# Kernel tuning notes

Hardware: AMD Instinct MI355X
Metric: run time of the kernel (lower is better)

Reference implementation:

```python
import jax, jax.numpy as jnp
import numpy as np

DIM = 1024
HEADS = 16
DIM_HEAD = 64
SCALE = DIM_HEAD ** -0.5
LN_EPS = 1e-5


def layer_norm(x, g, b):
    mu = jnp.mean(x, axis=-1, keepdims=True)
    var = jnp.mean(jnp.square(x - mu), axis=-1, keepdims=True)
    return (x - mu) * jax.lax.rsqrt(var + LN_EPS) * g + b


def setup_inputs() -> dict:
    key = jax.random.key(0)
    ks = jax.random.split(key, 8)
    w_std = DIM ** -0.5  # keep GEMM outputs O(1)
    return {
        "query": jax.random.normal(ks[0], (4, 512, DIM), jnp.float32),
        "kv": jax.random.normal(ks[1], (4, 2048, DIM), jnp.float32),
        "ln_q_g": jnp.ones((DIM,), jnp.float32),
        "ln_q_b": jnp.zeros((DIM,), jnp.float32),
        "ln_kv_g": jnp.ones((DIM,), jnp.float32),
        "ln_kv_b": jnp.zeros((DIM,), jnp.float32),
        "Wq": jax.random.normal(ks[2], (DIM, DIM), jnp.float32) * w_std,
        "bq": jnp.zeros((DIM,), jnp.float32),
        "Wk": jax.random.normal(ks[3], (DIM, DIM), jnp.float32) * w_std,
        "bk": jnp.zeros((DIM,), jnp.float32),
        "Wv": jax.random.normal(ks[4], (DIM, DIM), jnp.float32) * w_std,
        "bv": jnp.zeros((DIM,), jnp.float32),
        "Wo": jax.random.normal(ks[5], (DIM, DIM), jnp.float32) * w_std,
        "bo": jnp.zeros((DIM,), jnp.float32),
    }


def reference(query, kv, ln_q_g, ln_q_b, ln_kv_g, ln_kv_b,
              Wq, bq, Wk, bk, Wv, bv, Wo, bo):
    kv_n = layer_norm(kv, ln_kv_g, ln_kv_b)            # (b, n_kv, d)
    residual = query
    q_n = layer_norm(query, ln_q_g, ln_q_b)            # (b, n_q, d)

    q = q_n @ Wq + bq                                   # (b, n_q, inner)
    kv_input = jnp.concatenate((kv_n, q_n), axis=-2)    # (b, n_kv+n_q, d)
    k = kv_input @ Wk + bk
    v = kv_input @ Wv + bv

    def split_heads(t):
        b, n, _ = t.shape
        return t.reshape(b, n, HEADS, DIM_HEAD).transpose(0, 2, 1, 3)  # b h n dh

    q = split_heads(q) * SCALE
    k = split_heads(k)
    v = split_heads(v)

    sim = jnp.einsum('bhid,bhjd->bhij', q, k)           # (b, h, n_q, n_kv+n_q)
    sim = sim - jax.lax.stop_gradient(jnp.max(sim, axis=-1, keepdims=True))
    attn = jax.nn.softmax(sim, axis=-1)
    out = jnp.einsum('bhij,bhjd->bhid', attn, v)        # (b, h, n_q, dh)

    b, h, n, dh = out.shape
    out = out.transpose(0, 2, 1, 3).reshape(b, n, h * dh)
    return out @ Wo + bo + residual
```

## Files before the change

### kernel.cpp

```cpp
#include <hip/hip_runtime.h>
#include <hip/hip_bf16.h>

#define B_    4
#define NQ    512
#define NKV   2048
#define NT    2560
#define DIM_  1024
#define HEADS 16
#define DH    64
#define NSEQT 10240
#define SCALE_Q_L2E 0.18033688011112042f

typedef short bf16x8 __attribute__((ext_vector_type(8)));
typedef float f32x4  __attribute__((ext_vector_type(4)));
typedef __hip_bfloat16 bf16;

__device__ inline void gll16(const bf16* g, bf16* l) {
  __builtin_amdgcn_global_load_lds(
      (const __attribute__((address_space(1))) unsigned int*)g,
      (__attribute__((address_space(3))) unsigned int*)l, 16, 0, 0);
}

#define VMCNT(n) asm volatile("s_waitcnt vmcnt(" #n ")" ::: "memory")
#define BAR() __builtin_amdgcn_s_barrier()

__global__ __launch_bounds__(256) void prep2_kernel(
    const float* __restrict__ query, const float* __restrict__ kv,
    const float* __restrict__ lgq, const float* __restrict__ lbq,
    const float* __restrict__ lgkv, const float* __restrict__ lbkv,
    bf16* __restrict__ X,
    const float* __restrict__ W0, const float* __restrict__ W1,
    const float* __restrict__ W2, const float* __restrict__ W3,
    bf16* __restrict__ T0, bf16* __restrict__ T1,
    bf16* __restrict__ T2, bf16* __restrict__ T3)
{
  __shared__ __align__(16) char psm[9216];
  const int t = threadIdx.x;
  const int blkid = blockIdx.x;
  if (blkid < 2560) {
    const int w = t>>6, l = t&63;
    const int R = blkid*4 + w;
    int b = R / NT, r = R % NT;
    const float *src, *gp, *bp;
    if (r < NKV) { src = kv    + ((size_t)b*NKV + r)*DIM_;      gp = lgkv; bp = lbkv; }
    else         { src = query + ((size_t)b*NQ + (r-NKV))*DIM_; gp = lgq;  bp = lbq;  }
    float4 v[4];
    #pragma unroll
    for (int j=0;j<4;++j) v[j] = ((const float4*)src)[j*64 + l];
    float s = 0.f, s2 = 0.f;
    #pragma unroll
    for (int j=0;j<4;++j){
      s  += v[j].x+v[j].y+v[j].z+v[j].w;
      s2 += v[j].x*v[j].x+v[j].y*v[j].y+v[j].z*v[j].z+v[j].w*v[j].w;
    }
    #pragma unroll
    for (int m=1;m<64;m<<=1){ s += __shfl_xor(s,m,64); s2 += __shfl_xor(s2,m,64); }
    float mu = s*(1.0f/DIM_);
    float rs = rsqrtf(s2*(1.0f/DIM_) - mu*mu + 1e-5f);
    uint2* drow = (uint2*)(X + (size_t)R*DIM_);
    #pragma unroll
    for (int j=0;j<4;++j){
      float4 gg = ((const float4*)gp)[j*64 + l];
      float4 b4 = ((const float4*)bp)[j*64 + l];
      union { unsigned int u[2]; bf16 h[4]; } pk;
      pk.h[0] = __float2bfloat16((v[j].x-mu)*rs*gg.x + b4.x);
      pk.h[1] = __float2bfloat16((v[j].y-mu)*rs*gg.y + b4.y);
      pk.h[2] = __float2bfloat16((v[j].z-mu)*rs*gg.z + b4.z);
      pk.h[3] = __float2bfloat16((v[j].w-mu)*rs*gg.w + b4.w);
      drow[j*64 + l] = make_uint2(pk.u[0], pk.u[1]);
    }
  } else {
    int l = blkid - 2560;
    const float* W; bf16* Wt;
    switch (l>>8) {
      case 0: W=W0; Wt=T0; break;
      case 1: W=W1; Wt=T1; break;
      case 2: W=W2; Wt=T2; break;
      default: W=W3; Wt=T3; break;
    }
    int rem = l & 255;
    int k0 = (rem&15)*64, n0 = (rem>>4)*64;
    bf16* Ws = (bf16*)psm;
    int kr = t>>2, nseg = (t&3)*16;
    const float4* s4 = (const float4*)(W + (size_t)(k0+kr)*DIM_ + n0 + nseg);
    union { uint4 u[2]; bf16 h[16]; } pk;
    #pragma unroll
    for (int j=0;j<4;j++){
      float4 v = s4[j];
      pk.h[j*4+0]=__float2bfloat16(v.x); pk.h[j*4+1]=__float2bfloat16(v.y);
      pk.h[j*4+2]=__float2bfloat16(v.z); pk.h[j*4+3]=__float2bfloat16(v.w);
    }
    *(uint4*)(Ws + kr*72 + nseg)     = pk.u[0];
    *(uint4*)(Ws + kr*72 + nseg + 8) = pk.u[1];
    __syncthreads();
    int n = t&63, kseg = t>>6;
    union { uint4 u[2]; bf16 h[16]; } o;
    #pragma unroll
    for (int k=0;k<16;k++) o.h[k] = Ws[(kseg*16+k)*72 + n];
    bf16* dst = Wt + (size_t)(n0+n)*DIM_ + k0 + kseg*16;
    *(uint4*)dst = o.u[0];
    *(uint4*)(dst+8) = o.u[1];
  }
}

__device__ __forceinline__ void gemm_core3(
    const bf16* __restrict__ A, const bf16* __restrict__ Bmat,
    const float* __restrict__ bias, const float* __restrict__ residual,
    void* __restrict__ outv, int rows_per_batch, int row_offset,
    int a_batch_stride_rows, int n_seq, float scale,
    int emode, int m0, int n0, char* smem)
{
  char* const sA = smem;
  char* const sB = smem + 24576;
  float* Ts = (float*)smem;

  const int t = threadIdx.x;
  const int lrow = t>>3, sl = t&7;
  const int sp   = sl ^ (lrow & 7);
  const int hsel = sp>>2, g = sp&3;
  const bf16 *pA[2], *pB[2];
  #pragma unroll
  for (int c = 0; c < 2; ++c) {
    int gm = m0 + 32*c + lrow + 64*hsel;
    int bi = gm / rows_per_batch;
    pA[c] = A + ((size_t)bi*a_batch_stride_rows + row_offset
                 + (gm - bi*rows_per_batch))*(size_t)DIM_ + g*8;
    int gn = n0 + 32*c + lrow + 64*hsel;
    pB[c] = Bmat + (size_t)gn*(size_t)DIM_ + g*8;
  }
  const int toff = t*16;

  const int wave = t>>6, lane = t&63, qq = lane>>4, mr = lane&15;
  const int wm = (wave>>1)*64, wn = (wave&1)*64;
  const int sAo = ((((wm>>6)<<2)|qq) ^ (mr&7))*16 + mr*128;
  const int sBo = ((((wn>>6)<<2)|qq) ^ (mr&7))*16 + mr*128;

  f32x4 acc[4][4] = {};

  #pragma unroll
  for (int p = 0; p < 2; ++p) {
    const int ko = p*32, bo = p*8192;
    gll16(pA[0]+ko, (bf16*)(sA + bo + toff));
    gll16(pA[1]+ko, (bf16*)(sA + bo + 4096 + toff));
    gll16(pB[0]+ko, (bf16*)(sB + bo + toff));
    gll16(pB[1]+ko, (bf16*)(sB + bo + 4096 + toff));
  }

  int rd = 0, wr2 = 2;
  for (int kt = 0; kt < 32; ++kt) {
    {
      const int kt2 = (kt+2 < 32) ? kt+2 : 31;
      const int ko = kt2*32, bo = wr2*8192;
      gll16(pA[0]+ko, (bf16*)(sA + bo + toff));
      gll16(pA[1]+ko, (bf16*)(sA + bo + 4096 + toff));
      gll16(pB[0]+ko, (bf16*)(sB + bo + toff));
      gll16(pB[1]+ko, (bf16*)(sB + bo + 4096 + toff));
    }
    VMCNT(8);
    BAR();
    {
      const char* Ab = sA + rd*8192;
      const char* Bb = sB + rd*8192;
      bf16x8 af[4], bfr[4];
      #pragma unroll
      for (int ms=0; ms<4; ++ms) af[ms]  = *(const bf16x8*)(Ab + ms*2048 + sAo);
      #pragma unroll
      for (int ns=0; ns<4; ++ns) bfr[ns] = *(const bf16x8*)(Bb + ns*2048 + sBo);
      __builtin_amdgcn_s_setprio(1);
      #pragma unroll
      for (int ms=0; ms<4; ++ms)
        #pragma unroll
        for (int ns=0; ns<4; ++ns)
          acc[ms][ns] = __builtin_amdgcn_mfma_f32_16x16x32_bf16(
              af[ms], bfr[ns], acc[ms][ns], 0,0,0);
      __builtin_amdgcn_s_setprio(0);
    }
    BAR();
    rd  = (rd  == 2) ? 0 : rd  + 1;
    wr2 = (wr2 == 2) ? 0 : wr2 + 1;
  }
  VMCNT(0);
  __syncthreads();

  const int lr = t>>3, cs = (t&7)*16;
  for (int R=0; R<4; R++){
    if ((wave>>1) == (R>>1)) {
      #pragma unroll
      for (int ms2=0; ms2<2; ms2++){
        int ms = (R&1)*2 + ms2;
        #pragma unroll
        for (int ns=0; ns<4; ns++){
          int col = wn + ns*16 + mr;
          #pragma unroll
          for (int r=0;r<4;r++)
            Ts[(ms2*16 + qq*4 + r)*132 + col] = acc[ms][ns][r];
        }
      }
    }
    __syncthreads();
    float v[16];
    #pragma unroll
    for (int j=0;j<4;j++){
      float4 f = *(const float4*)(Ts + lr*132 + cs + j*4);
      v[j*4+0]=f.x; v[j*4+1]=f.y; v[j*4+2]=f.z; v[j*4+3]=f.w;
    }
    int gr = m0 + R*32 + lr;
    int gc = n0 + cs;
    if (emode == 0) {
      float* out = (float*)outv;
      size_t base = (size_t)gr*DIM_ + gc;
      #pragma unroll
      for (int j=0;j<4;j++){
        float4 bv = *(const float4*)(bias + gc + j*4);
        float4 rv = *(const float4*)(residual + base + j*4);
        float4 o4;
        o4.x = v[j*4+0] + bv.x + rv.x;
        o4.y = v[j*4+1] + bv.y + rv.y;
        o4.z = v[j*4+2] + bv.z + rv.z;
        o4.w = v[j*4+3] + bv.w + rv.w;
        *(float4*)(out + base + j*4) = o4;
      }
    } else if (emode == 1) {
      int bb = gr / rows_per_batch;
      int n  = gr - bb*rows_per_batch;
      int hh = gc>>6, dh = gc&63;
      bf16* out = (bf16*)outv + ((size_t)(bb*HEADS + hh)*n_seq + n)*DH + dh;
      union { uint4 u[2]; bf16 h[16]; } pk;
      #pragma unroll
      for (int j=0;j<16;j++) pk.h[j] = __float2bfloat16((v[j] + bias[gc+j])*scale);
      *(uint4*)out     = pk.u[0];
      *(uint4*)(out+8) = pk.u[1];
    } else {
      float bc = bias[gr];
      bf16* out = (bf16*)outv + (size_t)gr*NSEQT + gc;
      union { uint4 u[2]; bf16 h[16]; } pk;
      #pragma unroll
      for (int j=0;j<16;j++) pk.h[j] = __float2bfloat16(v[j] + bc);
      *(uint4*)out     = pk.u[0];
      *(uint4*)(out+8) = pk.u[1];
    }
    __syncthreads();
  }
}

__global__ __launch_bounds__(256, 3) void gemm_qkv4(
    const bf16* __restrict__ X,
    const bf16* __restrict__ WtQ, const bf16* __restrict__ WtK,
    const bf16* __restrict__ WtV,
    const float* __restrict__ bq, const float* __restrict__ bk,
    const float* __restrict__ bv,
    bf16* __restrict__ Qhb, bf16* __restrict__ Khb, bf16* __restrict__ VTg)
{
  __shared__ __align__(16) char smem[49152];
  const int blk = blockIdx.x;
  if (blk < 128) {
    gemm_core3(X, WtQ, bq, nullptr, Qhb, NQ, NKV, NT, NQ, SCALE_Q_L2E, 1,
               (blk&15)*128, (blk>>4)*128, smem);
  } else if (blk < 768) {
    int l = blk - 128;
    gemm_core3(X, WtK, bk, nullptr, Khb, NT, 0, NT, NT, 1.0f, 1,
               (l%80)*128, (l/80)*128, smem);
  } else {
    int l = blk - 768;
    gemm_core3(WtV, X, bv, nullptr, VTg, DIM_, 0, DIM_, NSEQT, 1.0f, 2,
               (l/80)*128, (l%80)*128, smem);
  }
}

__global__ __launch_bounds__(256, 3) void gemm_o(
    const bf16* __restrict__ Ctx, const bf16* __restrict__ WtO,
    const float* __restrict__ bo, const float* __restrict__ residual,
    float* __restrict__ out)
{
  __shared__ __align__(16) char smem[49152];
  const int blk = blockIdx.x;
  gemm_core3(Ctx, WtO, bo, residual, out, B_*NQ, 0, B_*NQ, NQ, 1.0f, 0,
             (blk&15)*128, (blk>>4)*128, smem);
}

__global__ __launch_bounds__(256) void attn6_kernel(
    const bf16* __restrict__ Qh, const bf16* __restrict__ Kh,
    const bf16* __restrict__ VTg, bf16* __restrict__ Ctx)
{
  __shared__ __align__(16) bf16 KV[2][8192];
  __shared__ __align__(16) unsigned int Ps[4][640];

  const int t = threadIdx.x, wave = t>>6, lane = t&63;
  const int qq = lane>>4, mr = lane&15;
  const int blk = blockIdx.x;
  const int bh = (blk&7)*8 + (blk>>6);
  const int q0 = ((blk>>3)&7)*64;
  const int b = bh>>4, h = bh&15;
  const int pair = wave>>1, kh = wave&1;
  const int qb = pair*32;

  const int sl = t>>2, sc = t&3;
  const int skey = 32*(sl>>5) + 2*(sl&15) + ((sl>>4)&1);
  const bf16* Kb  = Kh + (size_t)bh*NT*DH + (size_t)skey*DH + sc*8;
  const bf16* VbT = VTg + ((size_t)(h*DH) + sl)*NSEQT + (size_t)b*NT + sc*8;

  bf16x8 qf[2][2];
  #pragma unroll
  for (int mt=0; mt<2; mt++){
    const bf16* Qb = Qh + ((size_t)bh*NQ + q0 + qb + mt*16 + mr)*DH;
    qf[mt][0] = *(const bf16x8*)(Qb + qq*8);
    qf[mt][1] = *(const bf16x8*)(Qb + 32 + qq*8);
  }

  f32x4 o[2][4] = {};
  float l[2][4] = {};
  unsigned int* Pw = &Ps[wave][0];

  {
    bf16* bp = &KV[0][0];
    gll16(Kb,        bp + t*8);
    gll16(Kb + 32,   bp + 2048 + t*8);
    gll16(VbT,       bp + 4096 + t*8);
    gll16(VbT + 32,  bp + 6144 + t*8);
  }

  for (int it = 0; it < NT/64; it++) {
    __syncthreads();
    if (it + 1 < NT/64) {
      int kt = (it+1)*64;
      bf16* bp = &KV[(it+1)&1][0];
      gll16(Kb  + (size_t)kt*DH,      bp + t*8);
      gll16(Kb  + (size_t)kt*DH + 32, bp + 2048 + t*8);
      gll16(VbT + kt,                 bp + 4096 + t*8);
      gll16(VbT + kt + 32,            bp + 6144 + t*8);
    }
    const bf16* cbuf = &KV[it&1][0];

    bf16x8 kf[2][2];
    #pragma unroll
    for (int g=0; g<2; g++){
      kf[g][0] = *(const bf16x8*)(cbuf + (32*kh + 16*g + mr)*32 + qq*8);
      kf[g][1] = *(const bf16x8*)(cbuf + 2048 + (32*kh + 16*g + mr)*32 + qq*8);
    }
    f32x4 s[2][2];
    #pragma unroll
    for (int mt=0; mt<2; mt++)
      #pragma unroll
      for (int g=0; g<2; g++){
        f32x4 z = {};
        z = __builtin_amdgcn_mfma_f32_16x16x32_bf16(qf[mt][0], kf[g][0], z, 0,0,0);
        z = __builtin_amdgcn_mfma_f32_16x16x32_bf16(qf[mt][1], kf[g][1], z, 0,0,0);
        s[mt][g] = z;
      }
    bf16x8 vf[4];
    #pragma unroll
    for (int n2=0; n2<4; n2++)
      vf[n2] = *(const bf16x8*)(cbuf + 4096 + kh*2048 + (n2*16+mr)*32 + qq*8);

    #pragma unroll
    for (int mt=0; mt<2; mt++)
      #pragma unroll
      for (int r=0; r<4; r++){
        float e0 = __builtin_amdgcn_exp2f(s[mt][0][r]);
        float e1 = __builtin_amdgcn_exp2f(s[mt][1][r]);
        l[mt][r] += e0 + e1;
        unsigned a0 = __float_as_uint(e0) + 0x8000u;
        unsigned a1 = __float_as_uint(e1) + 0x8000u;
        Pw[(mt*16 + qq*4 + r)*20 + mr] = __builtin_amdgcn_perm(a1, a0, 0x07060302u);
      }
    asm volatile("s_waitcnt lgkmcnt(0)" ::: "memory");
    bf16x8 pa[2];
    #pragma unroll
    for (int mt=0; mt<2; mt++)
      pa[mt] = *(const bf16x8*)(Pw + (mt*16+mr)*20 + qq*4);
    #pragma unroll
    for (int mt=0; mt<2; mt++)
      #pragma unroll
      for (int n2=0; n2<4; n2++)
        o[mt][n2] = __builtin_amdgcn_mfma_f32_16x16x32_bf16(pa[mt], vf[n2], o[mt][n2], 0,0,0);
  }

  float lsum[2][4];
  #pragma unroll
  for (int mt=0; mt<2; mt++)
    #pragma unroll
    for (int r=0; r<4; r++){
      float v = l[mt][r];
      #pragma unroll
      for (int m=1;m<16;m<<=1) v += __shfl_xor(v, m, 16);
      lsum[mt][r] = v;
    }

  __syncthreads();
  float* Of  = (float*)&KV[0][0];
  float* lsh = (float*)&Ps[0][0];
  if (kh == 1) {
    #pragma unroll
    for (int mt=0; mt<2; mt++){
      #pragma unroll
      for (int n2=0; n2<4; n2++)
        #pragma unroll
        for (int r=0; r<4; r++)
          Of[(qb + mt*16 + qq*4 + r)*68 + n2*16 + mr] = o[mt][n2][r];
      if (mr == 0)
        #pragma unroll
        for (int r=0; r<4; r++)
          lsh[qb + mt*16 + qq*4 + r] = lsum[mt][r];
    }
  }
  __syncthreads();
  if (kh == 0) {
    #pragma unroll
    for (int mt=0; mt<2; mt++)
      #pragma unroll
      for (int r=0; r<4; r++){
        int row = qb + mt*16 + qq*4 + r;
        float rl = 1.0f / (lsum[mt][r] + lsh[row]);
        #pragma unroll
        for (int n2=0; n2<4; n2++){
          int idx = row*68 + n2*16 + mr;
          Of[idx] = (o[mt][n2][r] + Of[idx]) * rl;
        }
      }
  }
  __syncthreads();
  {
    int row = t>>2, seg = (t&3)*16;
    union { uint4 u[2]; bf16 hh[16]; } pkv;
    #pragma unroll
    for (int j=0;j<16;j++) pkv.hh[j] = __float2bfloat16(Of[row*68 + seg + j]);
    bf16* dst = Ctx + ((size_t)b*NQ + q0 + row)*DIM_ + h*DH + seg;
    *(uint4*)dst = pkv.u[0];
    *(uint4*)(dst+8) = pkv.u[1];
  }
}

extern "C" void kernel_launch(void* const* d_in, const int* in_sizes, int n_in,
                              void* d_out, int out_size, void* d_ws, size_t ws_size,
                              hipStream_t stream)
{
  const float* query  = (const float*)d_in[0];
  const float* kv     = (const float*)d_in[1];
  const float* ln_q_g = (const float*)d_in[2];
  const float* ln_q_b = (const float*)d_in[3];
  const float* ln_kv_g= (const float*)d_in[4];
  const float* ln_kv_b= (const float*)d_in[5];
  const float* Wq = (const float*)d_in[6];
  const float* bq = (const float*)d_in[7];
  const float* Wk = (const float*)d_in[8];
  const float* bk = (const float*)d_in[9];
  const float* Wv = (const float*)d_in[10];
  const float* bv = (const float*)d_in[11];
  const float* Wo = (const float*)d_in[12];
  const float* bo = (const float*)d_in[13];
  float* out = (float*)d_out;

  char* ws = (char*)d_ws;
  size_t off = 0;
  auto take = [&](size_t bytes)->char* {
    char* p = ws + off; off += (bytes + 255) & ~(size_t)255; return p;
  };
  bf16* X    = (bf16*)take((size_t)B_*NT*DIM_*2);
  bf16* Qhb  = (bf16*)take((size_t)B_*NQ*DIM_*2);
  bf16* Khb  = (bf16*)take((size_t)B_*NT*DIM_*2);
  bf16* VTg  = (bf16*)take((size_t)DIM_*NSEQT*2);
  bf16* Ctx  = (bf16*)take((size_t)B_*NQ*DIM_*2);
  bf16* WtQ  = (bf16*)take((size_t)DIM_*DIM_*2);
  bf16* WtK  = (bf16*)take((size_t)DIM_*DIM_*2);
  bf16* WtV  = (bf16*)take((size_t)DIM_*DIM_*2);
  bf16* WtO  = (bf16*)take((size_t)DIM_*DIM_*2);

  prep2_kernel<<<3584, 256, 0, stream>>>(
      query, kv, ln_q_g, ln_q_b, ln_kv_g, ln_kv_b, X,
      Wq, Wk, Wv, Wo, WtQ, WtK, WtV, WtO);

  gemm_qkv4<<<1408, 256, 0, stream>>>(X, WtQ, WtK, WtV, bq, bk, bv,
                                      Qhb, Khb, VTg);

  attn6_kernel<<<512, 256, 0, stream>>>(Qhb, Khb, VTg, Ctx);

  gemm_o<<<128, 256, 0, stream>>>(Ctx, WtO, bo, query, out);
}
```

Measured before the change: 240.0 us.

## Load GEMM B operand directly into registers, stage only A through LDS

The GEMM core now stages only the A tile through LDS, double-buffered with a K step of 64. Each wave loads its B fragments straight from global memory into registers, prefetching one step ahead. This halves LDS traffic and footprint, and halves the number of barriers per K. The cost is more VGPR pressure (the occupancy hint of 3 blocks is dropped) and B reads that are not shared across the two waves using the same columns.

```diff
diff --git a/kernel.cpp b/kernel.cpp
--- a/kernel.cpp
+++ b/kernel.cpp
@@ -103,7 +103,7 @@
   }
 }
 
-__device__ __forceinline__ void gemm_core3(
+__device__ __forceinline__ void gemm_core4(
     const bf16* __restrict__ A, const bf16* __restrict__ Bmat,
     const float* __restrict__ bias, const float* __restrict__ residual,
     void* __restrict__ outv, int rows_per_batch, int row_offset,
@@ -111,74 +111,83 @@
     int emode, int m0, int n0, char* smem)
 {
   char* const sA = smem;
-  char* const sB = smem + 24576;
   float* Ts = (float*)smem;
 
   const int t = threadIdx.x;
-  const int lrow = t>>3, sl = t&7;
-  const int sp   = sl ^ (lrow & 7);
-  const int hsel = sp>>2, g = sp&3;
-  const bf16 *pA[2], *pB[2];
-  #pragma unroll
-  for (int c = 0; c < 2; ++c) {
-    int gm = m0 + 32*c + lrow + 64*hsel;
+  const int srow = t >> 3;
+  const int gsw  = (t & 7) ^ (srow & 7);
+  const bf16* pA[4];
+  #pragma unroll
+  for (int c = 0; c < 4; ++c) {
+    int gm = m0 + c*32 + srow;
     int bi = gm / rows_per_batch;
     pA[c] = A + ((size_t)bi*a_batch_stride_rows + row_offset
-                 + (gm - bi*rows_per_batch))*(size_t)DIM_ + g*8;
-    int gn = n0 + 32*c + lrow + 64*hsel;
-    pB[c] = Bmat + (size_t)gn*(size_t)DIM_ + g*8;
+                 + (gm - bi*rows_per_batch))*(size_t)DIM_ + gsw*8;
   }
   const int toff = t*16;
 
   const int wave = t>>6, lane = t&63, qq = lane>>4, mr = lane&15;
   const int wm = (wave>>1)*64, wn = (wave&1)*64;
-  const int sAo = ((((wm>>6)<<2)|qq) ^ (mr&7))*16 + mr*128;
-  const int sBo = ((((wn>>6)<<2)|qq) ^ (mr&7))*16 + mr*128;
+  const int xq0 = (( qq    ) ^ (mr&7)) << 4;
+  const int xq1 = ((4 + qq ) ^ (mr&7)) << 4;
+
+  const bf16* pB[4];
+  #pragma unroll
+  for (int ns = 0; ns < 4; ++ns)
+    pB[ns] = Bmat + (size_t)(n0 + wn + ns*16 + mr)*(size_t)DIM_ + qq*8;
 
   f32x4 acc[4][4] = {};
-
-  #pragma unroll
-  for (int p = 0; p < 2; ++p) {
-    const int ko = p*32, bo = p*8192;
-    gll16(pA[0]+ko, (bf16*)(sA + bo + toff));
-    gll16(pA[1]+ko, (bf16*)(sA + bo + 4096 + toff));
-    gll16(pB[0]+ko, (bf16*)(sB + bo + toff));
-    gll16(pB[1]+ko, (bf16*)(sB + bo + 4096 + toff));
-  }
-
-  int rd = 0, wr2 = 2;
-  for (int kt = 0; kt < 32; ++kt) {
-    {
-      const int kt2 = (kt+2 < 32) ? kt+2 : 31;
-      const int ko = kt2*32, bo = wr2*8192;
-      gll16(pA[0]+ko, (bf16*)(sA + bo + toff));
-      gll16(pA[1]+ko, (bf16*)(sA + bo + 4096 + toff));
-      gll16(pB[0]+ko, (bf16*)(sB + bo + toff));
-      gll16(pB[1]+ko, (bf16*)(sB + bo + 4096 + toff));
-    }
-    VMCNT(8);
-    BAR();
-    {
-      const char* Ab = sA + rd*8192;
-      const char* Bb = sB + rd*8192;
-      bf16x8 af[4], bfr[4];
-      #pragma unroll
-      for (int ms=0; ms<4; ++ms) af[ms]  = *(const bf16x8*)(Ab + ms*2048 + sAo);
-      #pragma unroll
-      for (int ns=0; ns<4; ++ns) bfr[ns] = *(const bf16x8*)(Bb + ns*2048 + sBo);
-      __builtin_amdgcn_s_setprio(1);
-      #pragma unroll
-      for (int ms=0; ms<4; ++ms)
-        #pragma unroll
-        for (int ns=0; ns<4; ++ns)
-          acc[ms][ns] = __builtin_amdgcn_mfma_f32_16x16x32_bf16(
-              af[ms], bfr[ns], acc[ms][ns], 0,0,0);
-      __builtin_amdgcn_s_setprio(0);
-    }
-    BAR();
-    rd  = (rd  == 2) ? 0 : rd  + 1;
-    wr2 = (wr2 == 2) ? 0 : wr2 + 1;
-  }
+  bf16x8 bA[4][2], bB[4][2];
+
+  #pragma unroll
+  for (int c=0;c<4;++c) gll16(pA[c], (bf16*)(sA + c*4096 + toff));
+  __builtin_amdgcn_sched_barrier(0);
+  #pragma unroll
+  for (int ns=0;ns<4;++ns)
+    #pragma unroll
+    for (int kh=0;kh<2;++kh)
+      bA[ns][kh] = *(const bf16x8*)(pB[ns] + kh*32);
+  VMCNT(0);
+  BAR();
+
+#define GBODY(CB, NB, KON, BCUR, BNXT)                                         \
+  {                                                                            \
+    _Pragma("unroll")                                                          \
+    for (int c=0;c<4;++c) gll16(pA[c]+(KON), (bf16*)(sA + (NB) + c*4096 + toff)); \
+    __builtin_amdgcn_sched_barrier(0);                                         \
+    _Pragma("unroll")                                                          \
+    for (int ns=0;ns<4;++ns)                                                   \
+      _Pragma("unroll")                                                        \
+      for (int kh=0;kh<2;++kh)                                                 \
+        BNXT[ns][kh] = *(const bf16x8*)(pB[ns] + (KON) + kh*32);               \
+    _Pragma("unroll")                                                          \
+    for (int kh=0;kh<2;++kh){                                                  \
+      const int xq = kh ? xq1 : xq0;                                           \
+      bf16x8 af[4];                                                            \
+      _Pragma("unroll")                                                        \
+      for (int ms=0; ms<4; ++ms)                                               \
+        af[ms] = *(const bf16x8*)(sA + (CB) + (wm + ms*16 + mr)*128 + xq);     \
+      __builtin_amdgcn_s_setprio(1);                                           \
+      _Pragma("unroll")                                                        \
+      for (int ms=0; ms<4; ++ms)                                               \
+        _Pragma("unroll")                                                      \
+        for (int ns=0; ns<4; ++ns)                                             \
+          acc[ms][ns] = __builtin_amdgcn_mfma_f32_16x16x32_bf16(               \
+              af[ms], BCUR[ns][kh], acc[ms][ns], 0,0,0);                       \
+      __builtin_amdgcn_s_setprio(0);                                           \
+    }                                                                          \
+    VMCNT(8);                \
+    BAR();                                                                     \
+  }
+
+  for (int kt2 = 0; kt2 < 16; kt2 += 2) {
+    const int ko1 = (kt2+1)*64;
+    const int ko2 = ((kt2+2 < 16) ? kt2+2 : 15)*64;
+    GBODY(0,     16384, ko1, bA, bB);
+    GBODY(16384, 0,     ko2, bB, bA);
+  }
+#undef GBODY
+
   VMCNT(0);
   __syncthreads();
 
@@ -243,7 +252,7 @@
   }
 }
 
-__global__ __launch_bounds__(256, 3) void gemm_qkv4(
+__global__ __launch_bounds__(256) void gemm_qkv5(
     const bf16* __restrict__ X,
     const bf16* __restrict__ WtQ, const bf16* __restrict__ WtK,
     const bf16* __restrict__ WtV,
@@ -251,30 +260,30 @@
     const float* __restrict__ bv,
     bf16* __restrict__ Qhb, bf16* __restrict__ Khb, bf16* __restrict__ VTg)
 {
-  __shared__ __align__(16) char smem[49152];
+  __shared__ __align__(16) char smem[32768];
   const int blk = blockIdx.x;
   if (blk < 128) {
-    gemm_core3(X, WtQ, bq, nullptr, Qhb, NQ, NKV, NT, NQ, SCALE_Q_L2E, 1,
+    gemm_core4(X, WtQ, bq, nullptr, Qhb, NQ, NKV, NT, NQ, SCALE_Q_L2E, 1,
                (blk&15)*128, (blk>>4)*128, smem);
   } else if (blk < 768) {
     int l = blk - 128;
-    gemm_core3(X, WtK, bk, nullptr, Khb, NT, 0, NT, NT, 1.0f, 1,
+    gemm_core4(X, WtK, bk, nullptr, Khb, NT, 0, NT, NT, 1.0f, 1,
                (l%80)*128, (l/80)*128, smem);
   } else {
     int l = blk - 768;
-    gemm_core3(WtV, X, bv, nullptr, VTg, DIM_, 0, DIM_, NSEQT, 1.0f, 2,
+    gemm_core4(WtV, X, bv, nullptr, VTg, DIM_, 0, DIM_, NSEQT, 1.0f, 2,
                (l/80)*128, (l%80)*128, smem);
   }
 }
 
-__global__ __launch_bounds__(256, 3) void gemm_o(
+__global__ __launch_bounds__(256) void gemm_o(
     const bf16* __restrict__ Ctx, const bf16* __restrict__ WtO,
     const float* __restrict__ bo, const float* __restrict__ residual,
     float* __restrict__ out)
 {
-  __shared__ __align__(16) char smem[49152];
+  __shared__ __align__(16) char smem[32768];
   const int blk = blockIdx.x;
-  gemm_core3(Ctx, WtO, bo, residual, out, B_*NQ, 0, B_*NQ, NQ, 1.0f, 0,
+  gemm_core4(Ctx, WtO, bo, residual, out, B_*NQ, 0, B_*NQ, NQ, 1.0f, 0,
              (blk&15)*128, (blk>>4)*128, smem);
 }
 
@@ -469,7 +478,7 @@
       query, kv, ln_q_g, ln_q_b, ln_kv_g, ln_kv_b, X,
       Wq, Wk, Wv, Wo, WtQ, WtK, WtV, WtO);
 
-  gemm_qkv4<<<1408, 256, 0, stream>>>(X, WtQ, WtK, WtV, bq, bk, bv,
+  gemm_qkv5<<<1408, 256, 0, stream>>>(X, WtQ, WtK, WtV, bq, bk, bv,
                                       Qhb, Khb, VTg);
 
   attn6_kernel<<<512, 256, 0, stream>>>(Qhb, Khb, VTg, Ctx);
```

Measured after the change: 307.2 us. 1.28x slower.
